# Optimization experiments

Measured on AMD Instinct MI355X. Metric: run time of the kernel, lower is better.

Reference implementation:

```python
import jax, jax.numpy as jnp
import numpy as np
import math

D_MODEL = 1024
NHEAD = 16
K_DIM = D_MODEL // NHEAD
B, S = 2, 2048

def setup_inputs() -> dict:
    key = jax.random.key(0)
    ks = jax.random.split(key, 12)
    sc = 1.0 / math.sqrt(D_MODEL)
    inp = {
        'query': jax.random.normal(ks[0], (B, S, D_MODEL), jnp.float32),
        'key':   jax.random.normal(ks[1], (B, S, D_MODEL), jnp.float32),
        'value': jax.random.normal(ks[2], (B, S, D_MODEL), jnp.float32),
        'Wq': jax.random.normal(ks[3], (D_MODEL, D_MODEL), jnp.float32) * sc,
        'bq': jnp.zeros((D_MODEL,), jnp.float32),
        'Wk': jax.random.normal(ks[4], (D_MODEL, D_MODEL), jnp.float32) * sc,
        'bk': jnp.zeros((D_MODEL,), jnp.float32),
        'Wv': jax.random.normal(ks[5], (D_MODEL, D_MODEL), jnp.float32) * sc,
        'bv': jnp.zeros((D_MODEL,), jnp.float32),
        'Wo': jax.random.normal(ks[6], (D_MODEL, D_MODEL), jnp.float32) * sc,
        'bo': jnp.zeros((D_MODEL,), jnp.float32),
    }
    return inp

def reference(query, key, value, Wq, bq, Wk, bk, Wv, bv, Wo, bo):
    b, s, _ = query.shape
    # Linear projections (torch Linear: x @ W.T + b), split into heads -> [b, h, s, d]
    Q = (query @ Wq.T + bq).reshape(b, s, NHEAD, K_DIM).transpose(0, 2, 1, 3)
    K = (key   @ Wk.T + bk).reshape(b, s, NHEAD, K_DIM).transpose(0, 2, 1, 3)
    V = (value @ Wv.T + bv).reshape(b, s, NHEAD, K_DIM).transpose(0, 2, 1, 3)
    scores = jnp.einsum('bhqd,bhkd->bhqk', Q, K) / math.sqrt(K_DIM)
    attn = jax.nn.softmax(scores, axis=-1)  # dropout = identity (eval)
    out = jnp.einsum('bhqk,bhkd->bhqd', attn, V)
    out = out.transpose(0, 2, 1, 3).reshape(b, s, D_MODEL)
    out = out @ Wo.T + bo
    return (out, attn)
```

## Files before the change

### kernel.cpp

```cpp
#include <hip/hip_runtime.h>
#include <hip/hip_bf16.h>
#include <stdint.h>

#define S_LEN 2048
#define NB 2
#define NH 16
#define DM 1024
#define KDIM 64
#define MTOK (NB*S_LEN)

typedef __attribute__((ext_vector_type(8))) short bf16x8;
typedef __attribute__((ext_vector_type(4))) float f32x4;
typedef __attribute__((ext_vector_type(4))) unsigned short u16x4;
typedef __attribute__((ext_vector_type(8))) unsigned short u16x8;

#define AS1 __attribute__((address_space(1)))
#define AS3 __attribute__((address_space(3)))

__device__ __forceinline__ unsigned short f2bf(float f) {
  unsigned int u = __builtin_bit_cast(unsigned int, f);
  return (unsigned short)((u + 0x7fffu + ((u >> 16) & 1u)) >> 16);
}
__device__ __forceinline__ f32x4 mfma16(bf16x8 a, bf16x8 b, f32x4 c) {
  return __builtin_amdgcn_mfma_f32_16x16x32_bf16(a, b, c, 0, 0, 0);
}

struct CvtArgs {
  const float* src[7];
  unsigned short* dst[7];
  int n[7];
};

__global__ __launch_bounds__(256) void cvt_f32_bf16(CvtArgs a) {
  const int seg = blockIdx.y;
  const float* __restrict__ s = a.src[seg];
  unsigned short* __restrict__ d = a.dst[seg];
  const int n4 = a.n[seg] >> 2;
  const int stride = gridDim.x * blockDim.x;
  for (int i = blockIdx.x * blockDim.x + threadIdx.x; i < n4; i += stride) {
    const float4 v = reinterpret_cast<const float4*>(s)[i];
    u16x4 o;
    o[0] = f2bf(v.x); o[1] = f2bf(v.y); o[2] = f2bf(v.z); o[3] = f2bf(v.w);
    reinterpret_cast<u16x4*>(d)[i] = o;
  }
}

struct GemmArgs {
  const unsigned short* A[3];
  const unsigned short* W[3];
  const float* bias[3];
  void* dst[3];
  int mode[3];
};

__global__ __launch_bounds__(256, 2)
void gemm_pipe(GemmArgs ga)
{
  __shared__ __align__(16) char smem[32768];

  const int z = blockIdx.z;
  const unsigned short* __restrict__ A  = ga.A[z];
  const unsigned short* __restrict__ Bw = ga.W[z];
  const float* __restrict__ bias = ga.bias[z];
  void* __restrict__ dst = ga.dst[z];
  const int mode = ga.mode[z];

  const int t = threadIdx.x;
  const int w = t >> 6, l = t & 63;
  const int g = l >> 4, cl = l & 15;
  const int m0 = blockIdx.y * 128;
  const int n0 = blockIdx.x * 128;

  const unsigned short* Ag = A  + (size_t)(m0 + (t >> 2)) * DM + (t & 3) * 8;
  const unsigned short* Bg = Bw + (size_t)(n0 + (t >> 2)) * DM + (t & 3) * 8;

  const int wm = (w >> 1) * 64, wn = (w & 1) * 64;

  f32x4 acc[4][4];
  #pragma unroll
  for (int i = 0; i < 4; ++i)
    #pragma unroll
    for (int j = 0; j < 4; ++j) acc[i][j] = 0.f;

  #define STAGE(step) do {                                                          \
    AS3 char* _buf = (AS3 char*)smem + ((step) & 1) * 16384;                         \
    __builtin_amdgcn_global_load_lds((const AS1 void*)(Ag + (step)*32),              \
                                     (AS3 void*)(_buf + w*1024),          16, 0, 0); \
    __builtin_amdgcn_global_load_lds((const AS1 void*)(Ag + (step)*32 + 64*DM),      \
                                     (AS3 void*)(_buf + 4096 + w*1024),   16, 0, 0); \
    __builtin_amdgcn_global_load_lds((const AS1 void*)(Bg + (step)*32),              \
                                     (AS3 void*)(_buf + 8192 + w*1024),   16, 0, 0); \
    __builtin_amdgcn_global_load_lds((const AS1 void*)(Bg + (step)*32 + 64*DM),      \
                                     (AS3 void*)(_buf + 12288 + w*1024),  16, 0, 0); \
  } while (0)

  STAGE(0);
  for (int s = 0; s < 32; ++s) {
    if (s < 31) {
      STAGE(s + 1);
      asm volatile("s_waitcnt vmcnt(4)" ::: "memory");
    } else {
      asm volatile("s_waitcnt vmcnt(0)" ::: "memory");
    }
    __builtin_amdgcn_s_barrier();
    __builtin_amdgcn_sched_barrier(0);

    const AS3 unsigned short* bufA =
        (const AS3 unsigned short*)((AS3 char*)smem + (s & 1) * 16384);
    const AS3 unsigned short* bufB = bufA + 4096;
    bf16x8 af[4], bfv[4];
    #pragma unroll
    for (int i = 0; i < 4; ++i)
      af[i] = *(const AS3 bf16x8*)(bufA + (wm + 16*i + cl) * 32 + g*8);
    #pragma unroll
    for (int j = 0; j < 4; ++j)
      bfv[j] = *(const AS3 bf16x8*)(bufB + (wn + 16*j + cl) * 32 + g*8);
    #pragma unroll
    for (int i = 0; i < 4; ++i)
      #pragma unroll
      for (int j = 0; j < 4; ++j)
        acc[i][j] = mfma16(af[i], bfv[j], acc[i][j]);

    __builtin_amdgcn_sched_barrier(0);
    __builtin_amdgcn_s_barrier();
  }
  #undef STAGE

  if (mode == 1) {
    unsigned short* Cs = (unsigned short*)smem;
    __syncthreads();
    #pragma unroll
    for (int i = 0; i < 4; ++i) {
      #pragma unroll
      for (int j = 0; j < 4; ++j) {
        const int n = wn + 16*j + cl;
        const float bn = bias[n0 + n];
        const int u = (wm >> 2) + 4*i + g;
        const int us = u ^ (n & 31);
        u16x4 o;
        #pragma unroll
        for (int r = 0; r < 4; ++r) o[r] = f2bf(acc[i][j][r] + bn);
        *reinterpret_cast<u16x4*>(&Cs[n*128 + us*4]) = o;
      }
    }
    __syncthreads();
    {
      const int n = t >> 1, mh = (t & 1) * 64;
      const int ncol = n0 + n;
      const int h = ncol >> 6, d = ncol & (KDIM-1);
      const int b = m0 >> 11, s0 = m0 & (S_LEN-1);
      unsigned short* drow = (unsigned short*)dst
          + ((size_t)(b*NH + h)*KDIM + d)*S_LEN + s0 + mh;
      #pragma unroll
      for (int mm = 0; mm < 4; ++mm) {
        u16x4 v[4];
        #pragma unroll
        for (int k = 0; k < 4; ++k) {
          const int us = ((mh >> 2) + mm*4 + k) ^ (n & 31);
          v[k] = *reinterpret_cast<const u16x4*>(&Cs[n*128 + us*4]);
        }
        u16x8 w01, w23;
        #pragma unroll
        for (int e = 0; e < 4; ++e) {
          w01[e] = v[0][e]; w01[4+e] = v[1][e];
          w23[e] = v[2][e]; w23[4+e] = v[3][e];
        }
        *reinterpret_cast<u16x8*>(drow + mm*16)     = w01;
        *reinterpret_cast<u16x8*>(drow + mm*16 + 8) = w23;
      }
    }
  } else {
    #pragma unroll
    for (int i = 0; i < 4; ++i)
      #pragma unroll
      for (int j = 0; j < 4; ++j) {
        const int ncol = n0 + wn + 16*j + cl;
        const float bn = bias[ncol];
        #pragma unroll
        for (int r = 0; r < 4; ++r) {
          const int m = m0 + wm + 16*i + g*4 + r;
          const float v = acc[i][j][r] + bn;
          if (mode == 0) {
            const int b = m >> 11, sR = m & (S_LEN-1);
            const int h = ncol >> 6, d = ncol & (KDIM-1);
            ((unsigned short*)dst)[((size_t)(b*NH + h)*S_LEN + sR)*KDIM + d] = f2bf(v);
          } else {
            ((float*)dst)[(size_t)m * DM + ncol] = v;
          }
        }
      }
  }
}

__global__ __launch_bounds__(512, 4)
void attn_fused7(const unsigned short* __restrict__ Qh,
                 const unsigned short* __restrict__ Kh,
                 const unsigned short* __restrict__ Vt,
                 float* __restrict__ attn,
                 unsigned short* __restrict__ ctx)
{
  __shared__ __align__(16) char smem[75776];
  AS3 char* const KB = (AS3 char*)smem;
  AS3 char* const VB = (AS3 char*)smem + 32768;

  const int id  = blockIdx.x;
  const int swz = (id & 7) * 64 + (id >> 3);
  const int bh  = swz >> 4;
  const int q0  = (swz & 15) * 128;

  const int t = threadIdx.x, w = t >> 6, l = t & 63;
  const int g = l >> 4, cl = l & 15;
  AS3 char* const PBw = (AS3 char*)smem + 65536 + w * 1280;
  const int b = bh >> 4, h = bh & 15;

  const unsigned short* Qb = Qh + ((size_t)bh * S_LEN + q0 + w*16 + cl) * KDIM;
  const bf16x8 qf0 = *reinterpret_cast<const bf16x8*>(Qb + g*8);
  const bf16x8 qf1 = *reinterpret_cast<const bf16x8*>(Qb + 32 + g*8);

  const int rs = (w & 3)*8 + (l >> 3), js = l & 7;
  const unsigned short* pK = Kh + (size_t)bh*S_LEN*KDIM + (size_t)rs*KDIM
                                + (size_t)((js ^ (rs & 7)) * 8);
  const int dsv = (w & 3)*16 + (l >> 2), jv = l & 3;
  const int kst = (dsv & 3) ^ ((dsv >> 2) & 3);
  const unsigned short* pV = Vt + (size_t)bh*KDIM*S_LEN + (size_t)dsv*S_LEN
                                + (size_t)((jv ^ kst) * 8);

  const unsigned kvkey = (unsigned)((cl & 3) ^ ((cl >> 2) & 3));
  const unsigned koff0 = (unsigned)(cl*128 + ((g ^ (cl & 7)) << 4));
  const unsigned koff1 = (unsigned)(cl*128 + (((g + 4) ^ (cl & 7)) << 4));
  const float SC2 = 0.125f * 1.44269504f;

  #define STAGE_KV(ch) do { int _b = (ch) & 7;                                              \
    if (w < 4) __builtin_amdgcn_global_load_lds((const AS1 void*)(pK + (size_t)(ch)*2048),  \
                   (AS3 void*)(KB + _b*4096 + (w&3)*1024), 16, 0, 0);                       \
    else       __builtin_amdgcn_global_load_lds((const AS1 void*)(pV + (size_t)(ch)*32),    \
                   (AS3 void*)(VB + _b*4096 + (w&3)*1024), 16, 0, 0); } while (0)
  #define STAGE_K(ch) do { int _b = (ch) & 7;                                               \
    if (w < 4) __builtin_amdgcn_global_load_lds((const AS1 void*)(pK + (size_t)(ch)*2048),  \
                   (AS3 void*)(KB + _b*4096 + (w&3)*1024), 16, 0, 0); } while (0)

  float sa0 = 0.f, sa1 = 0.f, sa2 = 0.f, sa3 = 0.f;
  f32x4 accP[4];
  #pragma unroll
  for (int dt = 0; dt < 4; ++dt) accP[dt] = 0.f;

  for (int i = 0; i < 6; ++i) STAGE_KV(i);
  for (int c = 0; c < 64; ++c) {
    STAGE_KV(c + 6);
    asm volatile("s_waitcnt vmcnt(6)" ::: "memory");
    __builtin_amdgcn_s_barrier();
    __builtin_amdgcn_sched_barrier(0);
    AS3 const char* kb = KB + (c & 7) * 4096;
    AS3 const char* vb = VB + (c & 7) * 4096;
    #pragma unroll
    for (int s = 0; s < 2; ++s) {
      const bf16x8 k0 = *(const AS3 bf16x8*)(kb + s*2048 + koff0);
      const bf16x8 k1 = *(const AS3 bf16x8*)(kb + s*2048 + koff1);
      f32x4 acc = {0.f, 0.f, 0.f, 0.f};
      acc = mfma16(k0, qf0, acc);
      acc = mfma16(k1, qf1, acc);
      const float p0 = __builtin_exp2f(acc[0] * SC2);
      const float p1 = __builtin_exp2f(acc[1] * SC2);
      const float p2 = __builtin_exp2f(acc[2] * SC2);
      const float p3 = __builtin_exp2f(acc[3] * SC2);
      sa0 += p0; sa1 += p1; sa2 += p2; sa3 += p3;
      u16x4 pb;
      pb[0] = f2bf(p0); pb[1] = f2bf(p1); pb[2] = f2bf(p2); pb[3] = f2bf(p3);
      *(AS3 u16x4*)(PBw + cl*80 + s*32 + g*8) = pb;
    }
    const bf16x8 ap = *(const AS3 bf16x8*)(PBw + cl*80 + g*16);
    #pragma unroll
    for (int dt = 0; dt < 4; ++dt) {
      const bf16x8 bv = *(const AS3 bf16x8*)(vb + (dt*16 + cl)*64 + ((g ^ kvkey) << 4));
      accP[dt] = mfma16(ap, bv, accP[dt]);
    }
  }

  float ssum = (sa0 + sa1) + (sa2 + sa3);
  ssum += __shfl_xor(ssum, 16, 64);
  ssum += __shfl_xor(ssum, 32, 64);
  const float inv = 1.0f / ssum;

  #pragma unroll
  for (int r = 0; r < 4; ++r) {
    const float invq = __shfl(inv, g*4 + r, 64);
    const size_t row = (size_t)(b * S_LEN + q0 + w*16 + g*4 + r);
    #pragma unroll
    for (int dt = 0; dt < 4; ++dt)
      ctx[row * DM + h * KDIM + dt*16 + cl] = f2bf(accP[dt][r] * invq);
  }

  __syncthreads();

  float* const arow = attn + ((size_t)bh * S_LEN + q0 + w*16 + cl) * S_LEN + g*4;

  for (int i = 0; i < 6; ++i) STAGE_K(i);
  for (int c = 0; c < 64; ++c) {
    STAGE_K(c + 6);
    if (w < 4) {
      if (c < 6) asm volatile("s_waitcnt vmcnt(6)"  ::: "memory");
      else       asm volatile("s_waitcnt vmcnt(18)" ::: "memory");
    }
    __builtin_amdgcn_s_barrier();
    __builtin_amdgcn_sched_barrier(0);
    AS3 const char* kb = KB + (c & 7) * 4096;
    #pragma unroll
    for (int s = 0; s < 2; ++s) {
      const bf16x8 k0 = *(const AS3 bf16x8*)(kb + s*2048 + koff0);
      const bf16x8 k1 = *(const AS3 bf16x8*)(kb + s*2048 + koff1);
      f32x4 acc = {0.f, 0.f, 0.f, 0.f};
      acc = mfma16(k0, qf0, acc);
      acc = mfma16(k1, qf1, acc);
      f32x4 p;
      p[0] = __builtin_exp2f(acc[0] * SC2) * inv;
      p[1] = __builtin_exp2f(acc[1] * SC2) * inv;
      p[2] = __builtin_exp2f(acc[2] * SC2) * inv;
      p[3] = __builtin_exp2f(acc[3] * SC2) * inv;
      *reinterpret_cast<f32x4*>(arow + c*32 + s*16) = p;
    }
  }
  #undef STAGE_KV
  #undef STAGE_K
}

extern "C" void kernel_launch(void* const* d_in, const int* in_sizes, int n_in,
                              void* d_out, int out_size, void* d_ws, size_t ws_size,
                              hipStream_t stream)
{
  const float* q_in = (const float*)d_in[0];
  const float* k_in = (const float*)d_in[1];
  const float* v_in = (const float*)d_in[2];
  const float* Wq   = (const float*)d_in[3];
  const float* bq   = (const float*)d_in[4];
  const float* Wk   = (const float*)d_in[5];
  const float* bk   = (const float*)d_in[6];
  const float* Wv   = (const float*)d_in[7];
  const float* bv   = (const float*)d_in[8];
  const float* Wo   = (const float*)d_in[9];
  const float* bo   = (const float*)d_in[10];

  unsigned short* qbf  = (unsigned short*)d_ws;
  unsigned short* kbf  = qbf  + (size_t)MTOK*DM;
  unsigned short* vbf  = kbf  + (size_t)MTOK*DM;
  unsigned short* wqbf = vbf  + (size_t)MTOK*DM;
  unsigned short* wkbf = wqbf + (size_t)DM*DM;
  unsigned short* wvbf = wkbf + (size_t)DM*DM;
  unsigned short* wobf = wvbf + (size_t)DM*DM;
  unsigned short* Qhp  = wobf + (size_t)DM*DM;
  unsigned short* Khp  = Qhp  + (size_t)MTOK*DM;
  unsigned short* Vtp  = Khp  + (size_t)MTOK*DM;
  unsigned short* ctx  = Vtp  + (size_t)MTOK*DM;

  float* out0 = (float*)d_out;
  float* attn = out0 + (size_t)MTOK*DM;

  CvtArgs ca;
  ca.src[0] = q_in; ca.dst[0] = qbf;  ca.n[0] = MTOK*DM;
  ca.src[1] = k_in; ca.dst[1] = kbf;  ca.n[1] = MTOK*DM;
  ca.src[2] = v_in; ca.dst[2] = vbf;  ca.n[2] = MTOK*DM;
  ca.src[3] = Wq;   ca.dst[3] = wqbf; ca.n[3] = DM*DM;
  ca.src[4] = Wk;   ca.dst[4] = wkbf; ca.n[4] = DM*DM;
  ca.src[5] = Wv;   ca.dst[5] = wvbf; ca.n[5] = DM*DM;
  ca.src[6] = Wo;   ca.dst[6] = wobf; ca.n[6] = DM*DM;
  cvt_f32_bf16<<<dim3(512, 7), 256, 0, stream>>>(ca);

  GemmArgs gq;
  gq.A[0] = qbf;  gq.W[0] = wqbf; gq.bias[0] = bq; gq.dst[0] = Qhp; gq.mode[0] = 0;
  gq.A[1] = kbf;  gq.W[1] = wkbf; gq.bias[1] = bk; gq.dst[1] = Khp; gq.mode[1] = 0;
  gq.A[2] = vbf;  gq.W[2] = wvbf; gq.bias[2] = bv; gq.dst[2] = Vtp; gq.mode[2] = 1;
  gemm_pipe<<<dim3(8, 32, 3), 256, 0, stream>>>(gq);

  attn_fused7<<<dim3(512), 512, 0, stream>>>(Qhp, Khp, Vtp, attn, ctx);

  GemmArgs go;
  go.A[0] = ctx; go.W[0] = wobf; go.bias[0] = bo; go.dst[0] = out0; go.mode[0] = 2;
  go.A[1] = ctx; go.W[1] = wobf; go.bias[1] = bo; go.dst[1] = out0; go.mode[1] = 2;
  go.A[2] = ctx; go.W[2] = wobf; go.bias[2] = bo; go.dst[2] = out0; go.mode[2] = 2;
  gemm_pipe<<<dim3(8, 32, 1), 256, 0, stream>>>(go);
}
```

Before: 298.9 us.

## Split attention across KV among waves with register-held probabilities, single pass

Rewrites the attention kernel so each block handles 16 query rows and its 8 waves each cover a 256-key slice. Each wave keeps its probabilities in registers. Row sums are combined across waves through shared memory and partial outputs are merged with shared atomics. The attention matrix is written from the stored bf16 probabilities, which removes the second QK^T recompute pass and the LDS K/V staging, but it rounds the attn output to bf16 precision and adds 8x more blocks. The GEMM also gets an XCD-aware tile remap so neighbouring tiles share L2.

```diff
diff --git a/kernel.cpp b/kernel.cpp
--- a/kernel.cpp
+++ b/kernel.cpp
@@ -20,6 +20,10 @@
 __device__ __forceinline__ unsigned short f2bf(float f) {
   unsigned int u = __builtin_bit_cast(unsigned int, f);
   return (unsigned short)((u + 0x7fffu + ((u >> 16) & 1u)) >> 16);
+}
+__device__ __forceinline__ float bf2f(unsigned short h) {
+  unsigned int u = ((unsigned int)h) << 16;
+  return __builtin_bit_cast(float, u);
 }
 __device__ __forceinline__ f32x4 mfma16(bf16x8 a, bf16x8 b, f32x4 c) {
   return __builtin_amdgcn_mfma_f32_16x16x32_bf16(a, b, c, 0, 0, 0);
@@ -68,8 +72,11 @@
   const int t = threadIdx.x;
   const int w = t >> 6, l = t & 63;
   const int g = l >> 4, cl = l & 15;
-  const int m0 = blockIdx.y * 128;
-  const int n0 = blockIdx.x * 128;
+
+  const int L   = blockIdx.x + 8 * blockIdx.y;
+  const int xcd = L & 7, ix = L >> 3;
+  const int m0  = (xcd * 4 + (ix & 3)) * 128;
+  const int n0  = (ix >> 2) * 128;
 
   const unsigned short* Ag = A  + (size_t)(m0 + (t >> 2)) * DM + (t & 3) * 8;
   const unsigned short* Bg = Bw + (size_t)(n0 + (t >> 2)) * DM + (t & 3) * 8;
@@ -193,134 +200,141 @@
 }
 
 __global__ __launch_bounds__(512, 4)
-void attn_fused7(const unsigned short* __restrict__ Qh,
-                 const unsigned short* __restrict__ Kh,
-                 const unsigned short* __restrict__ Vt,
-                 float* __restrict__ attn,
-                 unsigned short* __restrict__ ctx)
+void attn_reg(const unsigned short* __restrict__ Qh,
+              const unsigned short* __restrict__ Kh,
+              const unsigned short* __restrict__ Vt,
+              float* __restrict__ attn,
+              unsigned short* __restrict__ ctx)
 {
-  __shared__ __align__(16) char smem[75776];
-  AS3 char* const KB = (AS3 char*)smem;
-  AS3 char* const VB = (AS3 char*)smem + 32768;
+  __shared__ float statL[8][16];
+  __shared__ float Obuf[16][68];
+  __shared__ __align__(16) char PB[8][1280];
 
   const int id  = blockIdx.x;
-  const int swz = (id & 7) * 64 + (id >> 3);
-  const int bh  = swz >> 4;
-  const int q0  = (swz & 15) * 128;
+  const int swz = (id & 7) * 512 + (id >> 3);
+  const int bh  = swz >> 7;
+  const int q0  = (swz & 127) * 16;
 
   const int t = threadIdx.x, w = t >> 6, l = t & 63;
   const int g = l >> 4, cl = l & 15;
-  AS3 char* const PBw = (AS3 char*)smem + 65536 + w * 1280;
-  const int b = bh >> 4, h = bh & 15;
-
-  const unsigned short* Qb = Qh + ((size_t)bh * S_LEN + q0 + w*16 + cl) * KDIM;
+  const int kv0 = w * 256;
+
+  for (int i = t; i < 16 * 68; i += 512) (&Obuf[0][0])[i] = 0.f;
+
+  const unsigned short* Qb = Qh + ((size_t)bh * S_LEN + q0 + cl) * KDIM;
   const bf16x8 qf0 = *reinterpret_cast<const bf16x8*>(Qb + g*8);
   const bf16x8 qf1 = *reinterpret_cast<const bf16x8*>(Qb + 32 + g*8);
 
-  const int rs = (w & 3)*8 + (l >> 3), js = l & 7;
-  const unsigned short* pK = Kh + (size_t)bh*S_LEN*KDIM + (size_t)rs*KDIM
-                                + (size_t)((js ^ (rs & 7)) * 8);
-  const int dsv = (w & 3)*16 + (l >> 2), jv = l & 3;
-  const int kst = (dsv & 3) ^ ((dsv >> 2) & 3);
-  const unsigned short* pV = Vt + (size_t)bh*KDIM*S_LEN + (size_t)dsv*S_LEN
-                                + (size_t)((jv ^ kst) * 8);
-
-  const unsigned kvkey = (unsigned)((cl & 3) ^ ((cl >> 2) & 3));
-  const unsigned koff0 = (unsigned)(cl*128 + ((g ^ (cl & 7)) << 4));
-  const unsigned koff1 = (unsigned)(cl*128 + (((g + 4) ^ (cl & 7)) << 4));
+  const unsigned short* Kit = Kh + (size_t)bh*S_LEN*KDIM
+                                 + (size_t)(kv0 + cl)*KDIM + g*8;
   const float SC2 = 0.125f * 1.44269504f;
 
-  #define STAGE_KV(ch) do { int _b = (ch) & 7;                                              \
-    if (w < 4) __builtin_amdgcn_global_load_lds((const AS1 void*)(pK + (size_t)(ch)*2048),  \
-                   (AS3 void*)(KB + _b*4096 + (w&3)*1024), 16, 0, 0);                       \
-    else       __builtin_amdgcn_global_load_lds((const AS1 void*)(pV + (size_t)(ch)*32),    \
-                   (AS3 void*)(VB + _b*4096 + (w&3)*1024), 16, 0, 0); } while (0)
-  #define STAGE_K(ch) do { int _b = (ch) & 7;                                               \
-    if (w < 4) __builtin_amdgcn_global_load_lds((const AS1 void*)(pK + (size_t)(ch)*2048),  \
-                   (AS3 void*)(KB + _b*4096 + (w&3)*1024), 16, 0, 0); } while (0)
-
+  bf16x8 kA0 = *reinterpret_cast<const bf16x8*>(Kit);
+  bf16x8 kA1 = *reinterpret_cast<const bf16x8*>(Kit + 32);
+  bf16x8 kB0 = *reinterpret_cast<const bf16x8*>(Kit + 16*KDIM);
+  bf16x8 kB1 = *reinterpret_cast<const bf16x8*>(Kit + 16*KDIM + 32);
+
+  u16x4 p[16];
   float sa0 = 0.f, sa1 = 0.f, sa2 = 0.f, sa3 = 0.f;
-  f32x4 accP[4];
-  #pragma unroll
-  for (int dt = 0; dt < 4; ++dt) accP[dt] = 0.f;
-
-  for (int i = 0; i < 6; ++i) STAGE_KV(i);
-  for (int c = 0; c < 64; ++c) {
-    STAGE_KV(c + 6);
-    asm volatile("s_waitcnt vmcnt(6)" ::: "memory");
-    __builtin_amdgcn_s_barrier();
-    __builtin_amdgcn_sched_barrier(0);
-    AS3 const char* kb = KB + (c & 7) * 4096;
-    AS3 const char* vb = VB + (c & 7) * 4096;
-    #pragma unroll
-    for (int s = 0; s < 2; ++s) {
-      const bf16x8 k0 = *(const AS3 bf16x8*)(kb + s*2048 + koff0);
-      const bf16x8 k1 = *(const AS3 bf16x8*)(kb + s*2048 + koff1);
-      f32x4 acc = {0.f, 0.f, 0.f, 0.f};
-      acc = mfma16(k0, qf0, acc);
-      acc = mfma16(k1, qf1, acc);
-      const float p0 = __builtin_exp2f(acc[0] * SC2);
-      const float p1 = __builtin_exp2f(acc[1] * SC2);
-      const float p2 = __builtin_exp2f(acc[2] * SC2);
-      const float p3 = __builtin_exp2f(acc[3] * SC2);
-      sa0 += p0; sa1 += p1; sa2 += p2; sa3 += p3;
-      u16x4 pb;
-      pb[0] = f2bf(p0); pb[1] = f2bf(p1); pb[2] = f2bf(p2); pb[3] = f2bf(p3);
-      *(AS3 u16x4*)(PBw + cl*80 + s*32 + g*8) = pb;
-    }
-    const bf16x8 ap = *(const AS3 bf16x8*)(PBw + cl*80 + g*16);
-    #pragma unroll
-    for (int dt = 0; dt < 4; ++dt) {
-      const bf16x8 bv = *(const AS3 bf16x8*)(vb + (dt*16 + cl)*64 + ((g ^ kvkey) << 4));
-      accP[dt] = mfma16(ap, bv, accP[dt]);
-    }
+  #pragma unroll
+  for (int s = 0; s < 16; ++s) {
+    const bf16x8 k0 = kA0, k1 = kA1;
+    kA0 = kB0; kA1 = kB1;
+    const unsigned short* nxt = Kit + (size_t)(s + 2) * 16 * KDIM;
+    kB0 = *reinterpret_cast<const bf16x8*>(nxt);
+    kB1 = *reinterpret_cast<const bf16x8*>(nxt + 32);
+    f32x4 acc = {0.f, 0.f, 0.f, 0.f};
+    acc = mfma16(k0, qf0, acc);
+    acc = mfma16(k1, qf1, acc);
+    const float p0 = __builtin_exp2f(acc[0] * SC2);
+    const float p1 = __builtin_exp2f(acc[1] * SC2);
+    const float p2 = __builtin_exp2f(acc[2] * SC2);
+    const float p3 = __builtin_exp2f(acc[3] * SC2);
+    sa0 += p0; sa1 += p1; sa2 += p2; sa3 += p3;
+    u16x4 pb;
+    pb[0] = f2bf(p0); pb[1] = f2bf(p1); pb[2] = f2bf(p2); pb[3] = f2bf(p3);
+    p[s] = pb;
   }
 
   float ssum = (sa0 + sa1) + (sa2 + sa3);
   ssum += __shfl_xor(ssum, 16, 64);
   ssum += __shfl_xor(ssum, 32, 64);
-  const float inv = 1.0f / ssum;
+  if (l < 16) statL[w][l] = ssum;
+  __syncthreads();
+
+  float inv;
+  {
+    float s0 = statL[0][cl] + statL[1][cl] + statL[2][cl] + statL[3][cl];
+    float s1 = statL[4][cl] + statL[5][cl] + statL[6][cl] + statL[7][cl];
+    inv = 1.0f / (s0 + s1);
+  }
+
+  AS3 char* const PBw = (AS3 char*)&PB[w][0];
+  const unsigned short* Vb = Vt + (size_t)bh*KDIM*S_LEN + kv0;
+
+  bf16x8 vp0, vp1, vp2, vp3;
+  {
+    const unsigned short* Vp = Vb + (size_t)cl * S_LEN + g*8;
+    vp0 = *reinterpret_cast<const bf16x8*>(Vp);
+    vp1 = *reinterpret_cast<const bf16x8*>(Vp + 16 * S_LEN);
+    vp2 = *reinterpret_cast<const bf16x8*>(Vp + 32 * S_LEN);
+    vp3 = *reinterpret_cast<const bf16x8*>(Vp + 48 * S_LEN);
+  }
+
+  f32x4 accP[4];
+  #pragma unroll
+  for (int dt = 0; dt < 4; ++dt) accP[dt] = 0.f;
+
+  #pragma unroll
+  for (int ch = 0; ch < 8; ++ch) {
+    *(AS3 u16x4*)(PBw + cl*80 + g*8)      = p[2*ch];
+    *(AS3 u16x4*)(PBw + cl*80 + 32 + g*8) = p[2*ch + 1];
+    const bf16x8 v0 = vp0, v1 = vp1, v2 = vp2, v3 = vp3;
+    {
+      const unsigned short* Vp = Vb + (size_t)cl * S_LEN + (ch + 1)*32 + g*8;
+      vp0 = *reinterpret_cast<const bf16x8*>(Vp);
+      vp1 = *reinterpret_cast<const bf16x8*>(Vp + 16 * S_LEN);
+      vp2 = *reinterpret_cast<const bf16x8*>(Vp + 32 * S_LEN);
+      vp3 = *reinterpret_cast<const bf16x8*>(Vp + 48 * S_LEN);
+    }
+    const bf16x8 ap = *(const AS3 bf16x8*)(PBw + cl*80 + g*16);
+    accP[0] = mfma16(ap, v0, accP[0]);
+    accP[1] = mfma16(ap, v1, accP[1]);
+    accP[2] = mfma16(ap, v2, accP[2]);
+    accP[3] = mfma16(ap, v3, accP[3]);
+  }
 
   #pragma unroll
   for (int r = 0; r < 4; ++r) {
     const float invq = __shfl(inv, g*4 + r, 64);
-    const size_t row = (size_t)(b * S_LEN + q0 + w*16 + g*4 + r);
     #pragma unroll
     for (int dt = 0; dt < 4; ++dt)
-      ctx[row * DM + h * KDIM + dt*16 + cl] = f2bf(accP[dt][r] * invq);
-  }
-
+      atomicAdd(&Obuf[g*4 + r][dt*16 + cl], accP[dt][r] * invq);
+  }
   __syncthreads();
 
-  float* const arow = attn + ((size_t)bh * S_LEN + q0 + w*16 + cl) * S_LEN + g*4;
-
-  for (int i = 0; i < 6; ++i) STAGE_K(i);
-  for (int c = 0; c < 64; ++c) {
-    STAGE_K(c + 6);
-    if (w < 4) {
-      if (c < 6) asm volatile("s_waitcnt vmcnt(6)"  ::: "memory");
-      else       asm volatile("s_waitcnt vmcnt(18)" ::: "memory");
-    }
-    __builtin_amdgcn_s_barrier();
-    __builtin_amdgcn_sched_barrier(0);
-    AS3 const char* kb = KB + (c & 7) * 4096;
-    #pragma unroll
-    for (int s = 0; s < 2; ++s) {
-      const bf16x8 k0 = *(const AS3 bf16x8*)(kb + s*2048 + koff0);
-      const bf16x8 k1 = *(const AS3 bf16x8*)(kb + s*2048 + koff1);
-      f32x4 acc = {0.f, 0.f, 0.f, 0.f};
-      acc = mfma16(k0, qf0, acc);
-      acc = mfma16(k1, qf1, acc);
-      f32x4 p;
-      p[0] = __builtin_exp2f(acc[0] * SC2) * inv;
-      p[1] = __builtin_exp2f(acc[1] * SC2) * inv;
-      p[2] = __builtin_exp2f(acc[2] * SC2) * inv;
-      p[3] = __builtin_exp2f(acc[3] * SC2) * inv;
-      *reinterpret_cast<f32x4*>(arow + c*32 + s*16) = p;
-    }
-  }
-  #undef STAGE_KV
-  #undef STAGE_K
+  if (t < 256) {
+    const int b = bh >> 4, h = bh & 15;
+    const int q = t >> 4, d0 = (t & 15) * 4;
+    u16x4 o;
+    o[0] = f2bf(Obuf[q][d0 + 0]);
+    o[1] = f2bf(Obuf[q][d0 + 1]);
+    o[2] = f2bf(Obuf[q][d0 + 2]);
+    o[3] = f2bf(Obuf[q][d0 + 3]);
+    *reinterpret_cast<u16x4*>(
+        ctx + ((size_t)(b * S_LEN + q0 + q)) * DM + h * KDIM + d0) = o;
+  }
+
+  float* const arow = attn + ((size_t)bh * S_LEN + q0 + cl) * S_LEN + kv0 + g*4;
+  #pragma unroll
+  for (int s = 0; s < 16; ++s) {
+    f32x4 o;
+    o[0] = bf2f((unsigned short)p[s][0]) * inv;
+    o[1] = bf2f((unsigned short)p[s][1]) * inv;
+    o[2] = bf2f((unsigned short)p[s][2]) * inv;
+    o[3] = bf2f((unsigned short)p[s][3]) * inv;
+    *reinterpret_cast<f32x4*>(arow + s*16) = o;
+  }
 }
 
 extern "C" void kernel_launch(void* const* d_in, const int* in_sizes, int n_in,
@@ -370,11 +384,9 @@
   gq.A[2] = vbf;  gq.W[2] = wvbf; gq.bias[2] = bv; gq.dst[2] = Vtp; gq.mode[2] = 1;
   gemm_pipe<<<dim3(8, 32, 3), 256, 0, stream>>>(gq);
 
-  attn_fused7<<<dim3(512), 512, 0, stream>>>(Qhp, Khp, Vtp, attn, ctx);
+  attn_reg<<<dim3(4096), 512, 0, stream>>>(Qhp, Khp, Vtp, attn, ctx);
 
   GemmArgs go;
   go.A[0] = ctx; go.W[0] = wobf; go.bias[0] = bo; go.dst[0] = out0; go.mode[0] = 2;
-  go.A[1] = ctx; go.W[1] = wobf; go.bias[1] = bo; go.dst[1] = out0; go.mode[1] = 2;
-  go.A[2] = ctx; go.W[2] = wobf; go.bias[2] = bo; go.dst[2] = out0; go.mode[2] = 2;
   gemm_pipe<<<dim3(8, 32, 1), 256, 0, stream>>>(go);
 }
```

New measurement: 440.5 us. 47.4% more time.

## Move PV product into second attention pass and remap GEMM blocks per XCD

Applied to the files above, without the earlier changes.

The attention kernel's first pass now computes only the softmax row sums. The P·V product moves into the second pass, where it reuses the normalized probabilities already computed for the attention-matrix write. This removes the duplicate bf16 conversion and LDS staging of P from the first pass, but the second pass now loads V tiles as well as K and carries more work per iteration. The GEMM also remaps block indices so that each XCD handles a contiguous group of M tiles, which is meant to improve L2 reuse.

```diff
diff --git a/kernel.cpp b/kernel.cpp
--- a/kernel.cpp
+++ b/kernel.cpp
@@ -68,8 +68,11 @@
   const int t = threadIdx.x;
   const int w = t >> 6, l = t & 63;
   const int g = l >> 4, cl = l & 15;
-  const int m0 = blockIdx.y * 128;
-  const int n0 = blockIdx.x * 128;
+
+  const int L   = blockIdx.x + 8 * blockIdx.y;
+  const int xcd = L & 7, ix = L >> 3;
+  const int m0  = (xcd * 4 + (ix & 3)) * 128;
+  const int n0  = (ix >> 2) * 128;
 
   const unsigned short* Ag = A  + (size_t)(m0 + (t >> 2)) * DM + (t & 3) * 8;
   const unsigned short* Bg = Bw + (size_t)(n0 + (t >> 2)) * DM + (t & 3) * 8;
@@ -193,7 +196,7 @@
 }
 
 __global__ __launch_bounds__(512, 4)
-void attn_fused7(const unsigned short* __restrict__ Qh,
+void attn_fused9(const unsigned short* __restrict__ Qh,
                  const unsigned short* __restrict__ Kh,
                  const unsigned short* __restrict__ Vt,
                  float* __restrict__ attn,
@@ -230,28 +233,24 @@
   const unsigned koff1 = (unsigned)(cl*128 + (((g + 4) ^ (cl & 7)) << 4));
   const float SC2 = 0.125f * 1.44269504f;
 
+  #define STAGE_K(ch) do { int _b = (ch) & 7;                                               \
+    if (w < 4) __builtin_amdgcn_global_load_lds((const AS1 void*)(pK + (size_t)(ch)*2048),  \
+                   (AS3 void*)(KB + _b*4096 + (w&3)*1024), 16, 0, 0); } while (0)
   #define STAGE_KV(ch) do { int _b = (ch) & 7;                                              \
     if (w < 4) __builtin_amdgcn_global_load_lds((const AS1 void*)(pK + (size_t)(ch)*2048),  \
                    (AS3 void*)(KB + _b*4096 + (w&3)*1024), 16, 0, 0);                       \
     else       __builtin_amdgcn_global_load_lds((const AS1 void*)(pV + (size_t)(ch)*32),    \
                    (AS3 void*)(VB + _b*4096 + (w&3)*1024), 16, 0, 0); } while (0)
-  #define STAGE_K(ch) do { int _b = (ch) & 7;                                               \
-    if (w < 4) __builtin_amdgcn_global_load_lds((const AS1 void*)(pK + (size_t)(ch)*2048),  \
-                   (AS3 void*)(KB + _b*4096 + (w&3)*1024), 16, 0, 0); } while (0)
 
   float sa0 = 0.f, sa1 = 0.f, sa2 = 0.f, sa3 = 0.f;
-  f32x4 accP[4];
-  #pragma unroll
-  for (int dt = 0; dt < 4; ++dt) accP[dt] = 0.f;
-
-  for (int i = 0; i < 6; ++i) STAGE_KV(i);
+
+  for (int i = 0; i < 6; ++i) STAGE_K(i);
   for (int c = 0; c < 64; ++c) {
-    STAGE_KV(c + 6);
-    asm volatile("s_waitcnt vmcnt(6)" ::: "memory");
+    STAGE_K(c + 6);
+    if (w < 4) asm volatile("s_waitcnt vmcnt(6)" ::: "memory");
     __builtin_amdgcn_s_barrier();
     __builtin_amdgcn_sched_barrier(0);
     AS3 const char* kb = KB + (c & 7) * 4096;
-    AS3 const char* vb = VB + (c & 7) * 4096;
     #pragma unroll
     for (int s = 0; s < 2; ++s) {
       const bf16x8 k0 = *(const AS3 bf16x8*)(kb + s*2048 + koff0);
@@ -259,20 +258,10 @@
       f32x4 acc = {0.f, 0.f, 0.f, 0.f};
       acc = mfma16(k0, qf0, acc);
       acc = mfma16(k1, qf1, acc);
-      const float p0 = __builtin_exp2f(acc[0] * SC2);
-      const float p1 = __builtin_exp2f(acc[1] * SC2);
-      const float p2 = __builtin_exp2f(acc[2] * SC2);
-      const float p3 = __builtin_exp2f(acc[3] * SC2);
-      sa0 += p0; sa1 += p1; sa2 += p2; sa3 += p3;
-      u16x4 pb;
-      pb[0] = f2bf(p0); pb[1] = f2bf(p1); pb[2] = f2bf(p2); pb[3] = f2bf(p3);
-      *(AS3 u16x4*)(PBw + cl*80 + s*32 + g*8) = pb;
-    }
-    const bf16x8 ap = *(const AS3 bf16x8*)(PBw + cl*80 + g*16);
-    #pragma unroll
-    for (int dt = 0; dt < 4; ++dt) {
-      const bf16x8 bv = *(const AS3 bf16x8*)(vb + (dt*16 + cl)*64 + ((g ^ kvkey) << 4));
-      accP[dt] = mfma16(ap, bv, accP[dt]);
+      sa0 += __builtin_exp2f(acc[0] * SC2);
+      sa1 += __builtin_exp2f(acc[1] * SC2);
+      sa2 += __builtin_exp2f(acc[2] * SC2);
+      sa3 += __builtin_exp2f(acc[3] * SC2);
     }
   }
 
@@ -281,29 +270,22 @@
   ssum += __shfl_xor(ssum, 32, 64);
   const float inv = 1.0f / ssum;
 
+  __syncthreads();
+
+  float* const arow = attn + ((size_t)bh * S_LEN + q0 + w*16 + cl) * S_LEN + g*4;
+  f32x4 accP[4];
   #pragma unroll
-  for (int r = 0; r < 4; ++r) {
-    const float invq = __shfl(inv, g*4 + r, 64);
-    const size_t row = (size_t)(b * S_LEN + q0 + w*16 + g*4 + r);
-    #pragma unroll
-    for (int dt = 0; dt < 4; ++dt)
-      ctx[row * DM + h * KDIM + dt*16 + cl] = f2bf(accP[dt][r] * invq);
-  }
-
-  __syncthreads();
-
-  float* const arow = attn + ((size_t)bh * S_LEN + q0 + w*16 + cl) * S_LEN + g*4;
-
-  for (int i = 0; i < 6; ++i) STAGE_K(i);
+  for (int dt = 0; dt < 4; ++dt) accP[dt] = 0.f;
+
+  for (int i = 0; i < 6; ++i) STAGE_KV(i);
   for (int c = 0; c < 64; ++c) {
-    STAGE_K(c + 6);
-    if (w < 4) {
-      if (c < 6) asm volatile("s_waitcnt vmcnt(6)"  ::: "memory");
-      else       asm volatile("s_waitcnt vmcnt(18)" ::: "memory");
-    }
+    STAGE_KV(c + 6);
+    if (c < 6) asm volatile("s_waitcnt vmcnt(6)"  ::: "memory");
+    else       asm volatile("s_waitcnt vmcnt(18)" ::: "memory");
     __builtin_amdgcn_s_barrier();
     __builtin_amdgcn_sched_barrier(0);
     AS3 const char* kb = KB + (c & 7) * 4096;
+    AS3 const char* vb = VB + (c & 7) * 4096;
     #pragma unroll
     for (int s = 0; s < 2; ++s) {
       const bf16x8 k0 = *(const AS3 bf16x8*)(kb + s*2048 + koff0);
@@ -317,10 +299,27 @@
       p[2] = __builtin_exp2f(acc[2] * SC2) * inv;
       p[3] = __builtin_exp2f(acc[3] * SC2) * inv;
       *reinterpret_cast<f32x4*>(arow + c*32 + s*16) = p;
-    }
-  }
+      u16x4 pb;
+      pb[0] = f2bf(p[0]); pb[1] = f2bf(p[1]); pb[2] = f2bf(p[2]); pb[3] = f2bf(p[3]);
+      *(AS3 u16x4*)(PBw + cl*80 + s*32 + g*8) = pb;
+    }
+    const bf16x8 ap = *(const AS3 bf16x8*)(PBw + cl*80 + g*16);
+    #pragma unroll
+    for (int dt = 0; dt < 4; ++dt) {
+      const bf16x8 bv = *(const AS3 bf16x8*)(vb + (dt*16 + cl)*64 + ((g ^ kvkey) << 4));
+      accP[dt] = mfma16(ap, bv, accP[dt]);
+    }
+  }
+  #undef STAGE_K
   #undef STAGE_KV
-  #undef STAGE_K
+
+  #pragma unroll
+  for (int r = 0; r < 4; ++r) {
+    const size_t row = (size_t)(b * S_LEN + q0 + w*16 + g*4 + r);
+    #pragma unroll
+    for (int dt = 0; dt < 4; ++dt)
+      ctx[row * DM + h * KDIM + dt*16 + cl] = f2bf(accP[dt][r]);
+  }
 }
 
 extern "C" void kernel_launch(void* const* d_in, const int* in_sizes, int n_in,
@@ -370,11 +369,9 @@
   gq.A[2] = vbf;  gq.W[2] = wvbf; gq.bias[2] = bv; gq.dst[2] = Vtp; gq.mode[2] = 1;
   gemm_pipe<<<dim3(8, 32, 3), 256, 0, stream>>>(gq);
 
-  attn_fused7<<<dim3(512), 512, 0, stream>>>(Qhp, Khp, Vtp, attn, ctx);
+  attn_fused9<<<dim3(512), 512, 0, stream>>>(Qhp, Khp, Vtp, attn, ctx);
 
   GemmArgs go;
   go.A[0] = ctx; go.W[0] = wobf; go.bias[0] = bo; go.dst[0] = out0; go.mode[0] = 2;
-  go.A[1] = ctx; go.W[1] = wobf; go.bias[1] = bo; go.dst[1] = out0; go.mode[1] = 2;
-  go.A[2] = ctx; go.W[2] = wobf; go.bias[2] = bo; go.dst[2] = out0; go.mode[2] = 2;
   gemm_pipe<<<dim3(8, 32, 1), 256, 0, stream>>>(go);
 }
```

Result: faster. 278.1 us (-7.0%).
